# Performance work log

Measured on AMD Instinct MI355X. Metric: run time of the kernel, lower is better.

## Reference

```python
import jax, jax.numpy as jnp
import numpy as np

N_NODES = 10000
N_EDGES = 320000
HIDDEN = 64
IN_NODE = 4
IN_EDGE = 2
N_LAYERS = 4
COORDS_WEIGHT = 1.0
EPS = 1e-8


def _linear_params(key, fan_in, fan_out, scale=None, bias=True):
    k1, k2 = jax.random.split(key)
    s = scale if scale is not None else 1.0 / np.sqrt(fan_in)
    w = jax.random.uniform(k1, (fan_in, fan_out), jnp.float32, -s, s)
    b = jax.random.uniform(k2, (fan_out,), jnp.float32, -s, s) if bias else None
    return w, b


def setup_inputs() -> dict:
    key = jax.random.key(0)
    ks = jax.random.split(key, 16)
    his = jax.random.normal(ks[0], (N_NODES, IN_NODE), jnp.float32)
    loc = jax.random.normal(ks[1], (N_NODES, 3), jnp.float32)
    vel = jax.random.normal(ks[2], (N_NODES, 3), jnp.float32)
    edges = jax.random.randint(ks[3], (2, N_EDGES), 0, N_NODES, jnp.int64)
    edge_attr = jax.random.normal(ks[4], (N_EDGES, IN_EDGE), jnp.float32)
    emb_w, emb_b = _linear_params(ks[5], IN_NODE, HIDDEN)
    # edge MLP: cat(h_i, h_j, radial, edge_attr) -> hidden -> hidden
    edge_in = 2 * HIDDEN + 1 + IN_EDGE
    edge_w1, edge_b1 = _linear_params(ks[6], edge_in, HIDDEN)
    edge_w2, edge_b2 = _linear_params(ks[7], HIDDEN, HIDDEN)
    # node MLP: cat(h, agg) -> hidden -> hidden
    node_w1, node_b1 = _linear_params(ks[8], 2 * HIDDEN, HIDDEN)
    node_w2, node_b2 = _linear_params(ks[9], HIDDEN, HIDDEN)
    # coord MLP: hidden -> hidden -> 1 (last layer xavier-small, no bias, as in EGNN)
    coord_w1, coord_b1 = _linear_params(ks[10], HIDDEN, HIDDEN)
    coord_w2 = jax.random.normal(ks[11], (HIDDEN, 1), jnp.float32) * 0.001
    # coord_mlp_vel: hidden -> hidden -> 1
    vel_w1, vel_b1 = _linear_params(ks[12], HIDDEN, HIDDEN)
    vel_w2, vel_b2 = _linear_params(ks[13], HIDDEN, 1)
    return dict(his=his, loc=loc, edges=edges, vel=vel, edge_attr=edge_attr,
                emb_w=emb_w, emb_b=emb_b,
                edge_w1=edge_w1, edge_b1=edge_b1, edge_w2=edge_w2, edge_b2=edge_b2,
                node_w1=node_w1, node_b1=node_b1, node_w2=node_w2, node_b2=node_b2,
                coord_w1=coord_w1, coord_b1=coord_b1, coord_w2=coord_w2,
                vel_w1=vel_w1, vel_b1=vel_b1, vel_w2=vel_w2, vel_b2=vel_b2)


def _segment_mean(data, seg, num_segments):
    s = jax.ops.segment_sum(data, seg, num_segments=num_segments)
    cnt = jax.ops.segment_sum(jnp.ones((data.shape[0], 1), data.dtype), seg, num_segments=num_segments)
    return s / jnp.clip(cnt, 1.0, None)


def _egcl_vel(h, row, col, coord, vel, init_vel, edge_attr, p):
    """One E_GCL_ERGN_vel call: equivariant message passing + 2nd-order update."""
    n = h.shape[0]
    coord_diff = coord[row] - coord[col]                       # [E,3]
    radial = jnp.sum(coord_diff * coord_diff, axis=-1, keepdims=True)  # [E,1]
    # edge model
    e_in = jnp.concatenate([h[row], h[col], radial, edge_attr], axis=-1)
    ef = jax.nn.silu(e_in @ p['edge_w1'] + p['edge_b1'])
    ef = jax.nn.silu(ef @ p['edge_w2'] + p['edge_b2'])         # [E,H]
    # coord (acceleration) model
    gate = jax.nn.silu(ef @ p['coord_w1'] + p['coord_b1']) @ p['coord_w2']  # [E,1]
    acc = _segment_mean(coord_diff * gate, row, n) * COORDS_WEIGHT          # [N,3]
    # velocity model (norm_vel=True: normalize initial velocity direction)
    iv = init_vel / (jnp.linalg.norm(init_vel, axis=-1, keepdims=True) + EPS)
    phi = jax.nn.silu(h @ p['vel_w1'] + p['vel_b1']) @ p['vel_w2'] + p['vel_b2']  # [N,1]
    vel_new = vel + acc + phi * iv
    coord_new = coord + vel_new
    # node model
    agg = jax.ops.segment_sum(ef, row, num_segments=n)         # [N,H]
    hn = jax.nn.silu(jnp.concatenate([h, agg], axis=-1) @ p['node_w1'] + p['node_b1'])
    hn = hn @ p['node_w2'] + p['node_b2']                      # recurrent=False
    return hn, coord_new, vel_new


def reference(his, loc, edges, vel, edge_attr,
              emb_w, emb_b,
              edge_w1, edge_b1, edge_w2, edge_b2,
              node_w1, node_b1, node_w2, node_b2,
              coord_w1, coord_b1, coord_w2,
              vel_w1, vel_b1, vel_w2, vel_b2):
    p = dict(edge_w1=edge_w1, edge_b1=edge_b1, edge_w2=edge_w2, edge_b2=edge_b2,
             node_w1=node_w1, node_b1=node_b1, node_w2=node_w2, node_b2=node_b2,
             coord_w1=coord_w1, coord_b1=coord_b1, coord_w2=coord_w2,
             vel_w1=vel_w1, vel_b1=vel_b1, vel_w2=vel_w2, vel_b2=vel_b2)
    row, col = edges[0], edges[1]
    his_e = his @ emb_w + emb_b                                # embedding
    hi, x, v = _egcl_vel(his_e, row, col, loc, vel, vel, edge_attr, p)
    h = his_e + hi                                             # residual accumulation
    for _ in range(1, N_LAYERS):                               # shared layer, n_layers iters
        hi, x, v = _egcl_vel(h, row, col, x, v, vel, edge_attr, p)
        h = h + hi
    return x, h, v


if __name__ == '__main__':
    out = reference(**setup_inputs())
    print([o.shape for o in out])
```

## Files before the change

kernel.cpp:

```cpp
#include <hip/hip_runtime.h>
#include <hip/hip_bf16.h>
#include <math.h>

#define N_NODES 10000
#define N_EDGES 320000
#define HID 64
#define N_LAYERS 4
#define EDGE_BLOCKS 1250
#define EDGE_TILES_PER_WAVE 4
#define N_TILES_NODE 625
#define ALD 72

typedef unsigned short ushort_t;
typedef unsigned int uint_t;
typedef __attribute__((ext_vector_type(8))) short short8;
typedef __attribute__((ext_vector_type(4))) float floatx4;

__device__ __forceinline__ float silu_f(float x) {
    return x * (1.0f / (1.0f + __expf(-x)));
}
__device__ __forceinline__ ushort_t f2bf(float f) {
    uint_t u = __float_as_uint(f);
    uint_t r = u + 0x7FFFu + ((u >> 16) & 1u);
    return (ushort_t)(r >> 16);
}
__device__ __forceinline__ float bf2f(ushort_t u) {
    return __uint_as_float(((uint_t)u) << 16);
}
__device__ __forceinline__ uint_t pk2bf(float a, float b) {
    __hip_bfloat162 t = __float22bfloat162_rn(float2{a, b});
    union { __hip_bfloat162 h; uint_t u; } cv; cv.h = t; return cv.u;
}

__global__ void init_kernel(const float* __restrict__ loc, const float* __restrict__ vel,
                            float* __restrict__ x, float* __restrict__ v, float* __restrict__ iv) {
    int i = blockIdx.x * blockDim.x + threadIdx.x;
    if (i >= N_NODES) return;
    float v0 = vel[3*i], v1 = vel[3*i+1], v2 = vel[3*i+2];
    float nrm = sqrtf(v0*v0 + v1*v1 + v2*v2) + 1e-8f;
    x[3*i] = loc[3*i]; x[3*i+1] = loc[3*i+1]; x[3*i+2] = loc[3*i+2];
    v[3*i] = v0; v[3*i+1] = v1; v[3*i+2] = v2;
    iv[3*i] = v0/nrm; iv[3*i+1] = v1/nrm; iv[3*i+2] = v2/nrm;
}

__global__ __launch_bounds__(64) void embed_kernel(const float* __restrict__ his,
                                                   const float* __restrict__ w,
                                                   const float* __restrict__ b,
                                                   float* __restrict__ h0,
                                                   ushort_t* __restrict__ hbf) {
    int i = blockIdx.x, l = threadIdx.x;
    float acc = b[l];
    #pragma unroll
    for (int k = 0; k < 4; ++k) acc += his[i*4+k] * w[k*HID+l];
    h0[i*HID+l] = acc;
    hbf[i*HID+l] = f2bf(acc);
}

__global__ void count_kernel(const int* __restrict__ erow, int* __restrict__ counts) {
    int e = blockIdx.x * blockDim.x + threadIdx.x;
    if (e < N_EDGES) atomicAdd(&counts[erow[e]], 1);
}

__global__ __launch_bounds__(256) void scan_kernel(const int* __restrict__ counts,
                                                   int* __restrict__ offs) {
    __shared__ int part[256];
    const int t = threadIdx.x;
    const int base = t * 40;
    int s0 = 0;
    for (int k = 0; k < 40; ++k) {
        int i = base + k;
        if (i < N_NODES) s0 += counts[i];
    }
    part[t] = s0;
    __syncthreads();
    for (int d = 1; d < 256; d <<= 1) {
        int vv = (t >= d) ? part[t-d] : 0;
        __syncthreads();
        part[t] += vv;
        __syncthreads();
    }
    int run = part[t] - s0;
    for (int k = 0; k < 40; ++k) {
        int i = base + k;
        if (i < N_NODES) { run += counts[i]; offs[i+1] = run; }
    }
    if (t == 0) offs[0] = 0;
}

__global__ void scatter_kernel(const int* __restrict__ erow, const int* __restrict__ ecol,
                               const float* __restrict__ eattr,
                               const int* __restrict__ offs,
                               int* __restrict__ cursor,
                               int* __restrict__ srow, int* __restrict__ scol,
                               float* __restrict__ seattr) {
    int e = blockIdx.x * blockDim.x + threadIdx.x;
    if (e < N_EDGES) {
        int r = erow[e];
        int p = atomicAdd(&cursor[r], 1);
        int pos = offs[r] + p;
        srow[pos] = r;
        scol[pos] = ecol[e];
        seattr[2*pos]   = eattr[2*e];
        seattr[2*pos+1] = eattr[2*e+1];
    }
}

__device__ __forceinline__ void pack_one(const float* __restrict__ src, ushort_t* __restrict__ dst,
                                         int u) {
    int kt = u >> 8, nt = (u >> 6) & 3, lane = u & 63;
    int quad = lane >> 4, lo = lane & 15;
    #pragma unroll
    for (int j = 0; j < 8; ++j) {
        int k = 32*kt + quad*8 + j, n = 16*nt + lo;
        dst[(size_t)u*8 + j] = f2bf(src[k*HID + n]);
    }
}
__global__ void pack_weights(const float* __restrict__ ew1, const float* __restrict__ ew2,
                             const float* __restrict__ cw1, const float* __restrict__ nw1,
                             const float* __restrict__ nw2, const float* __restrict__ vw1,
                             ushort_t* __restrict__ pw1, ushort_t* __restrict__ pw2,
                             ushort_t* __restrict__ pc1, ushort_t* __restrict__ pn1,
                             ushort_t* __restrict__ pn2, ushort_t* __restrict__ pv1) {
    int t = blockIdx.x * blockDim.x + threadIdx.x;
    if      (t < 1024) pack_one(ew1, pw1, t);
    else if (t < 1536) pack_one(ew2, pw2, t - 1024);
    else if (t < 2048) pack_one(cw1, pc1, t - 1536);
    else if (t < 3072) pack_one(nw1, pn1, t - 2048);
    else if (t < 3584) pack_one(nw2, pn2, t - 3072);
    else               pack_one(vw1, pv1, t - 3584);
}

__global__ __launch_bounds__(256, 4) void edge_kernel(
    const ushort_t* __restrict__ hbf, const float* __restrict__ x,
    const int* __restrict__ srow, const int* __restrict__ scol,
    const float* __restrict__ seattr,
    const float* __restrict__ ew1,
    const float* __restrict__ eb1, const float* __restrict__ eb2,
    const float* __restrict__ cb1, const float* __restrict__ cw2,
    const ushort_t* __restrict__ pw1, const ushort_t* __restrict__ pw2,
    const ushort_t* __restrict__ pc1,
    float* __restrict__ aggf, float* __restrict__ accf)
{
    __shared__ ushort_t sW1[4*4*64*8];
    __shared__ ushort_t sW2[2*4*64*8];
    __shared__ float sRW[3][HID];
    __shared__ float sB1[HID], sB2[HID], sCB1[HID], sCW2[HID];
    __shared__ ushort_t sAct[4][16*ALD];
    __shared__ float sEdge[4][16][8];

    const int wave = threadIdx.x >> 6, lane = threadIdx.x & 63;
    const int quad = lane >> 4, lo = lane & 15;

    short8 c1f[8];
    #pragma unroll
    for (int u = 0; u < 8; ++u)
        c1f[u] = *(const short8*)(pc1 + ((size_t)u*64 + lane)*8);

    for (int i = threadIdx.x; i < 4*4*64*8; i += 256) sW1[i] = pw1[i];
    for (int i = threadIdx.x; i < 2*4*64*8; i += 256) sW2[i] = pw2[i];
    for (int i = threadIdx.x; i < 3*HID; i += 256) sRW[i/HID][i%HID] = ew1[(128 + i/HID)*HID + (i%HID)];
    if (threadIdx.x < HID) {
        sB1[threadIdx.x]  = eb1[threadIdx.x];
        sB2[threadIdx.x]  = eb2[threadIdx.x];
        sCB1[threadIdx.x] = cb1[threadIdx.x];
        sCW2[threadIdx.x] = cw2[threadIdx.x];
    }
    __syncthreads();

    ushort_t* act = sAct[wave];
    float (*sed)[8] = sEdge[wave];

    int tile = blockIdx.x * 4 + wave;
    for (int it = 0; it < EDGE_TILES_PER_WAVE; ++it, tile += EDGE_BLOCKS*4) {
        const int p0 = tile * 16;
        const int rme = srow[p0 + lo], cme = scol[p0 + lo];
        if (lane < 16) {
            float d0 = x[3*rme]   - x[3*cme];
            float d1 = x[3*rme+1] - x[3*cme+1];
            float d2 = x[3*rme+2] - x[3*cme+2];
            const float2 ea = ((const float2*)seattr)[p0 + lane];
            sed[lane][0] = d0; sed[lane][1] = d1; sed[lane][2] = d2;
            sed[lane][3] = d0*d0 + d1*d1 + d2*d2;
            sed[lane][4] = ea.x; sed[lane][5] = ea.y;
        }
        const int nxt = __shfl(rme, (lane + 1) & 63, 64);
        unsigned long long bm = __ballot((lane < 16) && ((lane == 15) || (rme != nxt)));
        const uint_t bnd = (uint_t)(bm & 0xFFFFu);

        const ushort_t* hr = hbf + (size_t)rme * HID;
        const ushort_t* hc = hbf + (size_t)cme * HID;
        short8 af0 = *(const short8*)(hr + quad*8);
        short8 af1 = *(const short8*)(hr + 32 + quad*8);
        short8 af2 = *(const short8*)(hc + quad*8);
        short8 af3 = *(const short8*)(hc + 32 + quad*8);

        floatx4 acc[4];
        #pragma unroll
        for (int nt = 0; nt < 4; ++nt) {
            floatx4 a = {0.f, 0.f, 0.f, 0.f};
            a = __builtin_amdgcn_mfma_f32_16x16x32_bf16(af0, *(const short8*)(sW1 + ((0*4+nt)*64+lane)*8), a, 0, 0, 0);
            a = __builtin_amdgcn_mfma_f32_16x16x32_bf16(af1, *(const short8*)(sW1 + ((1*4+nt)*64+lane)*8), a, 0, 0, 0);
            a = __builtin_amdgcn_mfma_f32_16x16x32_bf16(af2, *(const short8*)(sW1 + ((2*4+nt)*64+lane)*8), a, 0, 0, 0);
            a = __builtin_amdgcn_mfma_f32_16x16x32_bf16(af3, *(const short8*)(sW1 + ((3*4+nt)*64+lane)*8), a, 0, 0, 0);
            acc[nt] = a;
        }
        float rad[4], ea0[4], ea1[4];
        #pragma unroll
        for (int r = 0; r < 4; ++r) {
            const int m = 4*quad + r;
            rad[r] = sed[m][3]; ea0[r] = sed[m][4]; ea1[r] = sed[m][5];
        }
        #pragma unroll
        for (int nt = 0; nt < 4; ++nt) {
            const int n = 16*nt + lo;
            const float w128 = sRW[0][n], w129 = sRW[1][n], w130 = sRW[2][n], b1 = sB1[n];
            float vv[4];
            #pragma unroll
            for (int r = 0; r < 4; ++r)
                vv[r] = silu_f(acc[nt][r] + rad[r]*w128 + ea0[r]*w129 + ea1[r]*w130 + b1);
            const uint_t p01 = pk2bf(vv[0], vv[1]);
            const uint_t p23 = pk2bf(vv[2], vv[3]);
            act[(4*quad + 0)*ALD + n] = (ushort_t)(p01 & 0xFFFFu);
            act[(4*quad + 1)*ALD + n] = (ushort_t)(p01 >> 16);
            act[(4*quad + 2)*ALD + n] = (ushort_t)(p23 & 0xFFFFu);
            act[(4*quad + 3)*ALD + n] = (ushort_t)(p23 >> 16);
        }

        short8 g0 = *(const short8*)(act + lo*ALD + quad*8);
        short8 g1 = *(const short8*)(act + lo*ALD + 32 + quad*8);
        floatx4 acc2[4];
        #pragma unroll
        for (int nt = 0; nt < 4; ++nt) {
            floatx4 a = {0.f, 0.f, 0.f, 0.f};
            a = __builtin_amdgcn_mfma_f32_16x16x32_bf16(g0, *(const short8*)(sW2 + ((0*4+nt)*64+lane)*8), a, 0, 0, 0);
            a = __builtin_amdgcn_mfma_f32_16x16x32_bf16(g1, *(const short8*)(sW2 + ((1*4+nt)*64+lane)*8), a, 0, 0, 0);
            acc2[nt] = a;
        }
        #pragma unroll
        for (int nt = 0; nt < 4; ++nt) {
            const int n = 16*nt + lo;
            const float b2 = sB2[n];
            float vv[4];
            #pragma unroll
            for (int r = 0; r < 4; ++r) vv[r] = silu_f(acc2[nt][r] + b2);
            const uint_t p01 = pk2bf(vv[0], vv[1]);
            const uint_t p23 = pk2bf(vv[2], vv[3]);
            act[(4*quad + 0)*ALD + n] = (ushort_t)(p01 & 0xFFFFu);
            act[(4*quad + 1)*ALD + n] = (ushort_t)(p01 >> 16);
            act[(4*quad + 2)*ALD + n] = (ushort_t)(p23 & 0xFFFFu);
            act[(4*quad + 3)*ALD + n] = (ushort_t)(p23 >> 16);
        }

        {
            float s = 0.f;
            #pragma unroll
            for (int m = 0; m < 16; ++m) {
                s += bf2f(act[m*ALD + lane]);
                if ((bnd >> m) & 1u) {
                    const int row = __shfl(rme, m, 64);
                    atomicAdd(&aggf[(size_t)row*HID + lane], s);
                    s = 0.f;
                }
            }
        }

        short8 q0 = *(const short8*)(act + lo*ALD + quad*8);
        short8 q1 = *(const short8*)(act + lo*ALD + 32 + quad*8);
        float gs[4] = {0.f, 0.f, 0.f, 0.f};
        #pragma unroll
        for (int nt = 0; nt < 4; ++nt) {
            floatx4 a = {0.f, 0.f, 0.f, 0.f};
            a = __builtin_amdgcn_mfma_f32_16x16x32_bf16(q0, c1f[0*4+nt], a, 0, 0, 0);
            a = __builtin_amdgcn_mfma_f32_16x16x32_bf16(q1, c1f[1*4+nt], a, 0, 0, 0);
            const int n = 16*nt + lo;
            const float cb = sCB1[n], cw = sCW2[n];
            #pragma unroll
            for (int r = 0; r < 4; ++r) gs[r] += silu_f(a[r] + cb) * cw;
        }
        #pragma unroll
        for (int off = 1; off < 16; off <<= 1) {
            #pragma unroll
            for (int r = 0; r < 4; ++r) gs[r] += __shfl_xor(gs[r], off, 64);
        }
        int rr[4];
        #pragma unroll
        for (int r = 0; r < 4; ++r) rr[r] = __shfl(rme, 4*quad + r, 64);
        if (lo < 3) {
            #pragma unroll
            for (int r = 0; r < 4; ++r) {
                const int m = 4*quad + r;
                atomicAdd(&accf[(size_t)rr[r]*3 + lo], sed[m][lo] * gs[r]);
            }
        }
        __syncthreads();
    }
}

__global__ __launch_bounds__(64) void node_kernel(
    const float* __restrict__ h_in, float* __restrict__ h_out, ushort_t* __restrict__ hbf,
    float* __restrict__ x, float* __restrict__ v, const float* __restrict__ iv,
    float* __restrict__ aggf, float* __restrict__ accf,
    const int* __restrict__ offs,
    const ushort_t* __restrict__ pn1, const ushort_t* __restrict__ pn2,
    const ushort_t* __restrict__ pv1,
    const float* __restrict__ nb1, const float* __restrict__ nb2,
    const float* __restrict__ vb1, const float* __restrict__ vb2,
    const float* __restrict__ vw2)
{
    __shared__ ushort_t t1[16*ALD];
    __shared__ float sPhi[16];

    const int lane = threadIdx.x;
    const int tile = blockIdx.x;
    const int quad = lane >> 4, lo = lane & 15;
    const int i0 = tile * 16;

    int ov = 0;
    if (lane < 17) ov = offs[i0 + lane];

    const ushort_t* hrow = hbf + (size_t)(i0 + lo) * HID;
    short8 af0 = *(const short8*)(hrow + quad*8);
    short8 af1 = *(const short8*)(hrow + 32 + quad*8);
    float* ag = aggf + (size_t)(i0 + lo) * HID + quad*8;
    short8 af2, af3;
    #pragma unroll
    for (int j = 0; j < 4; ++j) {
        const uint_t u2 = pk2bf(ag[2*j], ag[2*j+1]);
        const uint_t u3 = pk2bf(ag[32 + 2*j], ag[32 + 2*j+1]);
        af2[2*j] = (short)(u2 & 0xFFFFu); af2[2*j+1] = (short)(u2 >> 16);
        af3[2*j] = (short)(u3 & 0xFFFFu); af3[2*j+1] = (short)(u3 >> 16);
    }
    floatx4 z = {0.f, 0.f, 0.f, 0.f};
    *(floatx4*)(ag)        = z;
    *(floatx4*)(ag + 4)    = z;
    *(floatx4*)(ag + 32)   = z;
    *(floatx4*)(ag + 36)   = z;

    #pragma unroll
    for (int nt = 0; nt < 4; ++nt) {
        floatx4 a = {0.f, 0.f, 0.f, 0.f};
        a = __builtin_amdgcn_mfma_f32_16x16x32_bf16(af0, *(const short8*)(pn1 + ((size_t)(0*4+nt)*64+lane)*8), a, 0, 0, 0);
        a = __builtin_amdgcn_mfma_f32_16x16x32_bf16(af1, *(const short8*)(pn1 + ((size_t)(1*4+nt)*64+lane)*8), a, 0, 0, 0);
        a = __builtin_amdgcn_mfma_f32_16x16x32_bf16(af2, *(const short8*)(pn1 + ((size_t)(2*4+nt)*64+lane)*8), a, 0, 0, 0);
        a = __builtin_amdgcn_mfma_f32_16x16x32_bf16(af3, *(const short8*)(pn1 + ((size_t)(3*4+nt)*64+lane)*8), a, 0, 0, 0);
        const int n = 16*nt + lo;
        const float b1 = nb1[n];
        float vv[4];
        #pragma unroll
        for (int r = 0; r < 4; ++r) vv[r] = silu_f(a[r] + b1);
        const uint_t p01 = pk2bf(vv[0], vv[1]);
        const uint_t p23 = pk2bf(vv[2], vv[3]);
        t1[(4*quad + 0)*ALD + n] = (ushort_t)(p01 & 0xFFFFu);
        t1[(4*quad + 1)*ALD + n] = (ushort_t)(p01 >> 16);
        t1[(4*quad + 2)*ALD + n] = (ushort_t)(p23 & 0xFFFFu);
        t1[(4*quad + 3)*ALD + n] = (ushort_t)(p23 >> 16);
    }

    short8 g0 = *(const short8*)(t1 + lo*ALD + quad*8);
    short8 g1 = *(const short8*)(t1 + lo*ALD + 32 + quad*8);
    #pragma unroll
    for (int nt = 0; nt < 4; ++nt) {
        floatx4 a = {0.f, 0.f, 0.f, 0.f};
        a = __builtin_amdgcn_mfma_f32_16x16x32_bf16(g0, *(const short8*)(pn2 + ((size_t)(0*4+nt)*64+lane)*8), a, 0, 0, 0);
        a = __builtin_amdgcn_mfma_f32_16x16x32_bf16(g1, *(const short8*)(pn2 + ((size_t)(1*4+nt)*64+lane)*8), a, 0, 0, 0);
        const int n = 16*nt + lo;
        const float b2 = nb2[n];
        #pragma unroll
        for (int r = 0; r < 4; ++r) {
            const int i = i0 + 4*quad + r;
            const float hnew = h_in[(size_t)i*HID + n] + a[r] + b2;
            h_out[(size_t)i*HID + n] = hnew;
            hbf[(size_t)i*HID + n] = f2bf(hnew);
        }
    }

    float gs[4] = {0.f, 0.f, 0.f, 0.f};
    #pragma unroll
    for (int nt = 0; nt < 4; ++nt) {
        floatx4 a = {0.f, 0.f, 0.f, 0.f};
        a = __builtin_amdgcn_mfma_f32_16x16x32_bf16(af0, *(const short8*)(pv1 + ((size_t)(0*4+nt)*64+lane)*8), a, 0, 0, 0);
        a = __builtin_amdgcn_mfma_f32_16x16x32_bf16(af1, *(const short8*)(pv1 + ((size_t)(1*4+nt)*64+lane)*8), a, 0, 0, 0);
        const int n = 16*nt + lo;
        const float b1 = vb1[n], w2 = vw2[n];
        #pragma unroll
        for (int r = 0; r < 4; ++r) gs[r] += silu_f(a[r] + b1) * w2;
    }
    #pragma unroll
    for (int off = 1; off < 16; off <<= 1) {
        #pragma unroll
        for (int r = 0; r < 4; ++r) gs[r] += __shfl_xor(gs[r], off, 64);
    }
    const float vb2s = vb2[0];
    if (lo == 0) {
        #pragma unroll
        for (int r = 0; r < 4; ++r) sPhi[4*quad + r] = gs[r] + vb2s;
    }

    if (lane < 48) {
        const int m = lane / 3, d = lane - m*3;
        const int s = __shfl(ov, m, 64), t = __shfl(ov, m + 1, 64);
        const int cnt = t - s;
        const int i = i0 + m;
        const float accm = accf[(size_t)i*3 + d] / (float)(cnt > 0 ? cnt : 1);
        accf[(size_t)i*3 + d] = 0.f;
        const float phi = sPhi[m];
        const float vn = v[3*i + d] + accm + phi * iv[3*i + d];
        v[3*i + d] = vn;
        x[3*i + d] += vn;
    }
}

__global__ void out_kernel(const float* __restrict__ x, const float* __restrict__ h,
                           const float* __restrict__ v, float* __restrict__ out) {
    int j = blockIdx.x * blockDim.x + threadIdx.x;
    const int nx = 3*N_NODES, nh = HID*N_NODES;
    if (j >= nx + nh + nx) return;
    if (j < nx) out[j] = x[j];
    else if (j < nx + nh) out[j] = h[j - nx];
    else out[j] = v[j - nx - nh];
}

extern "C" void kernel_launch(void* const* d_in, const int* in_sizes, int n_in,
                              void* d_out, int out_size, void* d_ws, size_t ws_size,
                              hipStream_t stream) {
    const float* his   = (const float*)d_in[0];
    const float* loc   = (const float*)d_in[1];
    const int*   edges = (const int*)  d_in[2];
    const float* vel   = (const float*)d_in[3];
    const float* eattr = (const float*)d_in[4];
    const float* emb_w = (const float*)d_in[5];
    const float* emb_b = (const float*)d_in[6];
    const float* ew1 = (const float*)d_in[7];
    const float* eb1 = (const float*)d_in[8];
    const float* ew2 = (const float*)d_in[9];
    const float* eb2 = (const float*)d_in[10];
    const float* nw1 = (const float*)d_in[11];
    const float* nb1 = (const float*)d_in[12];
    const float* nw2 = (const float*)d_in[13];
    const float* nb2 = (const float*)d_in[14];
    const float* cw1 = (const float*)d_in[15];
    const float* cb1 = (const float*)d_in[16];
    const float* cw2 = (const float*)d_in[17];
    const float* vw1 = (const float*)d_in[18];
    const float* vb1 = (const float*)d_in[19];
    const float* vw2 = (const float*)d_in[20];
    const float* vb2 = (const float*)d_in[21];

    const int* erow = edges;
    const int* ecol = edges + N_EDGES;

    char* ws = (char*)d_ws;
    size_t off = 0;
    auto walloc = [&](size_t bytes) -> void* {
        void* p = ws + off; off += (bytes + 255) & ~(size_t)255; return p;
    };
    float* h_a      = (float*)walloc((size_t)N_NODES*HID*4);
    float* h_b      = (float*)walloc((size_t)N_NODES*HID*4);
    ushort_t* hbf   = (ushort_t*)walloc((size_t)N_NODES*HID*2);
    float* xb       = (float*)walloc((size_t)N_NODES*3*4);
    float* vb       = (float*)walloc((size_t)N_NODES*3*4);
    float* ivb      = (float*)walloc((size_t)N_NODES*3*4);
    float* aggf     = (float*)walloc((size_t)N_NODES*HID*4);
    float* accf     = (float*)walloc((size_t)N_NODES*3*4);
    int* counts     = (int*)walloc((size_t)N_NODES*4);
    int* cursor     = (int*)walloc((size_t)N_NODES*4);
    int* offs       = (int*)walloc((size_t)(N_NODES+1)*4);
    int* srow       = (int*)walloc((size_t)N_EDGES*4);
    int* scol       = (int*)walloc((size_t)N_EDGES*4);
    float* seattr   = (float*)walloc((size_t)N_EDGES*2*4);
    ushort_t* pw1   = (ushort_t*)walloc((size_t)4*4*64*8*2);
    ushort_t* pw2   = (ushort_t*)walloc((size_t)2*4*64*8*2);
    ushort_t* pc1   = (ushort_t*)walloc((size_t)2*4*64*8*2);
    ushort_t* pn1   = (ushort_t*)walloc((size_t)4*4*64*8*2);
    ushort_t* pn2   = (ushort_t*)walloc((size_t)2*4*64*8*2);
    ushort_t* pv1   = (ushort_t*)walloc((size_t)2*4*64*8*2);

    (void)hipMemsetAsync(counts, 0, (size_t)N_NODES*4, stream);
    (void)hipMemsetAsync(cursor, 0, (size_t)N_NODES*4, stream);
    (void)hipMemsetAsync(aggf, 0, (size_t)N_NODES*HID*4, stream);
    (void)hipMemsetAsync(accf, 0, (size_t)N_NODES*3*4, stream);

    init_kernel<<<(N_NODES+255)/256, 256, 0, stream>>>(loc, vel, xb, vb, ivb);
    embed_kernel<<<N_NODES, 64, 0, stream>>>(his, emb_w, emb_b, h_a, hbf);
    count_kernel<<<(N_EDGES+255)/256, 256, 0, stream>>>(erow, counts);
    scan_kernel<<<1, 256, 0, stream>>>(counts, offs);
    scatter_kernel<<<(N_EDGES+255)/256, 256, 0, stream>>>(erow, ecol, eattr, offs, cursor,
                                                          srow, scol, seattr);
    pack_weights<<<16, 256, 0, stream>>>(ew1, ew2, cw1, nw1, nw2, vw1,
                                         pw1, pw2, pc1, pn1, pn2, pv1);

    float* h_cur = h_a;
    float* h_nxt = h_b;
    for (int layer = 0; layer < N_LAYERS; ++layer) {
        edge_kernel<<<EDGE_BLOCKS, 256, 0, stream>>>(hbf, xb, srow, scol, seattr,
                                                     ew1, eb1, eb2, cb1, cw2,
                                                     pw1, pw2, pc1, aggf, accf);
        node_kernel<<<N_TILES_NODE, 64, 0, stream>>>(h_cur, h_nxt, hbf, xb, vb, ivb,
                                                     aggf, accf, offs,
                                                     pn1, pn2, pv1,
                                                     nb1, nb2, vb1, vb2, vw2);
        float* tmp = h_cur; h_cur = h_nxt; h_nxt = tmp;
    }
    const int total = 3*N_NODES + HID*N_NODES + 3*N_NODES;
    out_kernel<<<(total+255)/256, 256, 0, stream>>>(xb, h_cur, vb, (float*)d_out);
}
```

Baseline: 499.1 us.

## Keep W2 in registers, raise edge occupancy, fuse init and output kernels

The edge kernel now holds the second-layer weights in per-lane registers instead of LDS, which shrinks shared memory. It raises the launch-bounds occupancy hint to 5 and pads the grid to 1280 blocks, adding a bounds guard per tile. Separately, the init kernel is merged into the embedding kernel, and the final node kernel writes x, h and v straight into the output buffer, so the out_kernel copy is gone. The cost is higher register pressure in the edge kernel, and some waves do no work because of the padded grid.

Result: slower. 542.3 us (+8.6%).

```diff
diff --git a/kernel.cpp b/kernel.cpp
--- a/kernel.cpp
+++ b/kernel.cpp
@@ -6,8 +6,9 @@
 #define N_EDGES 320000
 #define HID 64
 #define N_LAYERS 4
-#define EDGE_BLOCKS 1250
+#define EDGE_BLOCKS 1280
 #define EDGE_TILES_PER_WAVE 4
+#define N_TILES_EDGE 20000
 #define N_TILES_NODE 625
 #define ALD 72
 
@@ -32,28 +33,28 @@
     union { __hip_bfloat162 h; uint_t u; } cv; cv.h = t; return cv.u;
 }
 
-__global__ void init_kernel(const float* __restrict__ loc, const float* __restrict__ vel,
-                            float* __restrict__ x, float* __restrict__ v, float* __restrict__ iv) {
-    int i = blockIdx.x * blockDim.x + threadIdx.x;
-    if (i >= N_NODES) return;
-    float v0 = vel[3*i], v1 = vel[3*i+1], v2 = vel[3*i+2];
-    float nrm = sqrtf(v0*v0 + v1*v1 + v2*v2) + 1e-8f;
-    x[3*i] = loc[3*i]; x[3*i+1] = loc[3*i+1]; x[3*i+2] = loc[3*i+2];
-    v[3*i] = v0; v[3*i+1] = v1; v[3*i+2] = v2;
-    iv[3*i] = v0/nrm; iv[3*i+1] = v1/nrm; iv[3*i+2] = v2/nrm;
-}
-
 __global__ __launch_bounds__(64) void embed_kernel(const float* __restrict__ his,
+                                                   const float* __restrict__ loc,
+                                                   const float* __restrict__ vel,
                                                    const float* __restrict__ w,
                                                    const float* __restrict__ b,
                                                    float* __restrict__ h0,
-                                                   ushort_t* __restrict__ hbf) {
+                                                   ushort_t* __restrict__ hbf,
+                                                   float* __restrict__ x, float* __restrict__ v,
+                                                   float* __restrict__ iv) {
     int i = blockIdx.x, l = threadIdx.x;
     float acc = b[l];
     #pragma unroll
     for (int k = 0; k < 4; ++k) acc += his[i*4+k] * w[k*HID+l];
     h0[i*HID+l] = acc;
     hbf[i*HID+l] = f2bf(acc);
+    if (l == 0) {
+        float v0 = vel[3*i], v1 = vel[3*i+1], v2 = vel[3*i+2];
+        float nrm = sqrtf(v0*v0 + v1*v1 + v2*v2) + 1e-8f;
+        x[3*i] = loc[3*i]; x[3*i+1] = loc[3*i+1]; x[3*i+2] = loc[3*i+2];
+        v[3*i] = v0; v[3*i+1] = v1; v[3*i+2] = v2;
+        iv[3*i] = v0/nrm; iv[3*i+1] = v1/nrm; iv[3*i+2] = v2/nrm;
+    }
 }
 
 __global__ void count_kernel(const int* __restrict__ erow, int* __restrict__ counts) {
@@ -130,7 +131,7 @@
     else               pack_one(vw1, pv1, t - 3584);
 }
 
-__global__ __launch_bounds__(256, 4) void edge_kernel(
+__global__ __launch_bounds__(256, 5) void edge_kernel(
     const ushort_t* __restrict__ hbf, const float* __restrict__ x,
     const int* __restrict__ srow, const int* __restrict__ scol,
     const float* __restrict__ seattr,
@@ -142,7 +143,6 @@
     float* __restrict__ aggf, float* __restrict__ accf)
 {
     __shared__ ushort_t sW1[4*4*64*8];
-    __shared__ ushort_t sW2[2*4*64*8];
     __shared__ float sRW[3][HID];
     __shared__ float sB1[HID], sB2[HID], sCB1[HID], sCW2[HID];
     __shared__ ushort_t sAct[4][16*ALD];
@@ -151,13 +151,14 @@
     const int wave = threadIdx.x >> 6, lane = threadIdx.x & 63;
     const int quad = lane >> 4, lo = lane & 15;
 
-    short8 c1f[8];
-    #pragma unroll
-    for (int u = 0; u < 8; ++u)
+    short8 w2f[8], c1f[8];
+    #pragma unroll
+    for (int u = 0; u < 8; ++u) {
+        w2f[u] = *(const short8*)(pw2 + ((size_t)u*64 + lane)*8);
         c1f[u] = *(const short8*)(pc1 + ((size_t)u*64 + lane)*8);
+    }
 
     for (int i = threadIdx.x; i < 4*4*64*8; i += 256) sW1[i] = pw1[i];
-    for (int i = threadIdx.x; i < 2*4*64*8; i += 256) sW2[i] = pw2[i];
     for (int i = threadIdx.x; i < 3*HID; i += 256) sRW[i/HID][i%HID] = ew1[(128 + i/HID)*HID + (i%HID)];
     if (threadIdx.x < HID) {
         sB1[threadIdx.x]  = eb1[threadIdx.x];
@@ -172,124 +173,126 @@
 
     int tile = blockIdx.x * 4 + wave;
     for (int it = 0; it < EDGE_TILES_PER_WAVE; ++it, tile += EDGE_BLOCKS*4) {
-        const int p0 = tile * 16;
-        const int rme = srow[p0 + lo], cme = scol[p0 + lo];
-        if (lane < 16) {
-            float d0 = x[3*rme]   - x[3*cme];
-            float d1 = x[3*rme+1] - x[3*cme+1];
-            float d2 = x[3*rme+2] - x[3*cme+2];
-            const float2 ea = ((const float2*)seattr)[p0 + lane];
-            sed[lane][0] = d0; sed[lane][1] = d1; sed[lane][2] = d2;
-            sed[lane][3] = d0*d0 + d1*d1 + d2*d2;
-            sed[lane][4] = ea.x; sed[lane][5] = ea.y;
-        }
-        const int nxt = __shfl(rme, (lane + 1) & 63, 64);
-        unsigned long long bm = __ballot((lane < 16) && ((lane == 15) || (rme != nxt)));
-        const uint_t bnd = (uint_t)(bm & 0xFFFFu);
-
-        const ushort_t* hr = hbf + (size_t)rme * HID;
-        const ushort_t* hc = hbf + (size_t)cme * HID;
-        short8 af0 = *(const short8*)(hr + quad*8);
-        short8 af1 = *(const short8*)(hr + 32 + quad*8);
-        short8 af2 = *(const short8*)(hc + quad*8);
-        short8 af3 = *(const short8*)(hc + 32 + quad*8);
-
-        floatx4 acc[4];
-        #pragma unroll
-        for (int nt = 0; nt < 4; ++nt) {
-            floatx4 a = {0.f, 0.f, 0.f, 0.f};
-            a = __builtin_amdgcn_mfma_f32_16x16x32_bf16(af0, *(const short8*)(sW1 + ((0*4+nt)*64+lane)*8), a, 0, 0, 0);
-            a = __builtin_amdgcn_mfma_f32_16x16x32_bf16(af1, *(const short8*)(sW1 + ((1*4+nt)*64+lane)*8), a, 0, 0, 0);
-            a = __builtin_amdgcn_mfma_f32_16x16x32_bf16(af2, *(const short8*)(sW1 + ((2*4+nt)*64+lane)*8), a, 0, 0, 0);
-            a = __builtin_amdgcn_mfma_f32_16x16x32_bf16(af3, *(const short8*)(sW1 + ((3*4+nt)*64+lane)*8), a, 0, 0, 0);
-            acc[nt] = a;
-        }
-        float rad[4], ea0[4], ea1[4];
-        #pragma unroll
-        for (int r = 0; r < 4; ++r) {
-            const int m = 4*quad + r;
-            rad[r] = sed[m][3]; ea0[r] = sed[m][4]; ea1[r] = sed[m][5];
-        }
-        #pragma unroll
-        for (int nt = 0; nt < 4; ++nt) {
-            const int n = 16*nt + lo;
-            const float w128 = sRW[0][n], w129 = sRW[1][n], w130 = sRW[2][n], b1 = sB1[n];
-            float vv[4];
-            #pragma unroll
-            for (int r = 0; r < 4; ++r)
-                vv[r] = silu_f(acc[nt][r] + rad[r]*w128 + ea0[r]*w129 + ea1[r]*w130 + b1);
-            const uint_t p01 = pk2bf(vv[0], vv[1]);
-            const uint_t p23 = pk2bf(vv[2], vv[3]);
-            act[(4*quad + 0)*ALD + n] = (ushort_t)(p01 & 0xFFFFu);
-            act[(4*quad + 1)*ALD + n] = (ushort_t)(p01 >> 16);
-            act[(4*quad + 2)*ALD + n] = (ushort_t)(p23 & 0xFFFFu);
-            act[(4*quad + 3)*ALD + n] = (ushort_t)(p23 >> 16);
-        }
-
-        short8 g0 = *(const short8*)(act + lo*ALD + quad*8);
-        short8 g1 = *(const short8*)(act + lo*ALD + 32 + quad*8);
-        floatx4 acc2[4];
-        #pragma unroll
-        for (int nt = 0; nt < 4; ++nt) {
-            floatx4 a = {0.f, 0.f, 0.f, 0.f};
-            a = __builtin_amdgcn_mfma_f32_16x16x32_bf16(g0, *(const short8*)(sW2 + ((0*4+nt)*64+lane)*8), a, 0, 0, 0);
-            a = __builtin_amdgcn_mfma_f32_16x16x32_bf16(g1, *(const short8*)(sW2 + ((1*4+nt)*64+lane)*8), a, 0, 0, 0);
-            acc2[nt] = a;
-        }
-        #pragma unroll
-        for (int nt = 0; nt < 4; ++nt) {
-            const int n = 16*nt + lo;
-            const float b2 = sB2[n];
-            float vv[4];
-            #pragma unroll
-            for (int r = 0; r < 4; ++r) vv[r] = silu_f(acc2[nt][r] + b2);
-            const uint_t p01 = pk2bf(vv[0], vv[1]);
-            const uint_t p23 = pk2bf(vv[2], vv[3]);
-            act[(4*quad + 0)*ALD + n] = (ushort_t)(p01 & 0xFFFFu);
-            act[(4*quad + 1)*ALD + n] = (ushort_t)(p01 >> 16);
-            act[(4*quad + 2)*ALD + n] = (ushort_t)(p23 & 0xFFFFu);
-            act[(4*quad + 3)*ALD + n] = (ushort_t)(p23 >> 16);
-        }
-
-        {
-            float s = 0.f;
-            #pragma unroll
-            for (int m = 0; m < 16; ++m) {
-                s += bf2f(act[m*ALD + lane]);
-                if ((bnd >> m) & 1u) {
-                    const int row = __shfl(rme, m, 64);
-                    atomicAdd(&aggf[(size_t)row*HID + lane], s);
-                    s = 0.f;
-                }
-            }
-        }
-
-        short8 q0 = *(const short8*)(act + lo*ALD + quad*8);
-        short8 q1 = *(const short8*)(act + lo*ALD + 32 + quad*8);
-        float gs[4] = {0.f, 0.f, 0.f, 0.f};
-        #pragma unroll
-        for (int nt = 0; nt < 4; ++nt) {
-            floatx4 a = {0.f, 0.f, 0.f, 0.f};
-            a = __builtin_amdgcn_mfma_f32_16x16x32_bf16(q0, c1f[0*4+nt], a, 0, 0, 0);
-            a = __builtin_amdgcn_mfma_f32_16x16x32_bf16(q1, c1f[1*4+nt], a, 0, 0, 0);
-            const int n = 16*nt + lo;
-            const float cb = sCB1[n], cw = sCW2[n];
-            #pragma unroll
-            for (int r = 0; r < 4; ++r) gs[r] += silu_f(a[r] + cb) * cw;
-        }
-        #pragma unroll
-        for (int off = 1; off < 16; off <<= 1) {
-            #pragma unroll
-            for (int r = 0; r < 4; ++r) gs[r] += __shfl_xor(gs[r], off, 64);
-        }
-        int rr[4];
-        #pragma unroll
-        for (int r = 0; r < 4; ++r) rr[r] = __shfl(rme, 4*quad + r, 64);
-        if (lo < 3) {
+        if (tile < N_TILES_EDGE) {
+            const int p0 = tile * 16;
+            const int rme = srow[p0 + lo], cme = scol[p0 + lo];
+            if (lane < 16) {
+                float d0 = x[3*rme]   - x[3*cme];
+                float d1 = x[3*rme+1] - x[3*cme+1];
+                float d2 = x[3*rme+2] - x[3*cme+2];
+                const float2 ea = ((const float2*)seattr)[p0 + lane];
+                sed[lane][0] = d0; sed[lane][1] = d1; sed[lane][2] = d2;
+                sed[lane][3] = d0*d0 + d1*d1 + d2*d2;
+                sed[lane][4] = ea.x; sed[lane][5] = ea.y;
+            }
+            const int nxt = __shfl(rme, (lane + 1) & 63, 64);
+            unsigned long long bm = __ballot((lane < 16) && ((lane == 15) || (rme != nxt)));
+            const uint_t bnd = (uint_t)(bm & 0xFFFFu);
+
+            const ushort_t* hr = hbf + (size_t)rme * HID;
+            const ushort_t* hc = hbf + (size_t)cme * HID;
+            short8 af0 = *(const short8*)(hr + quad*8);
+            short8 af1 = *(const short8*)(hr + 32 + quad*8);
+            short8 af2 = *(const short8*)(hc + quad*8);
+            short8 af3 = *(const short8*)(hc + 32 + quad*8);
+
+            floatx4 acc[4];
+            #pragma unroll
+            for (int nt = 0; nt < 4; ++nt) {
+                floatx4 a = {0.f, 0.f, 0.f, 0.f};
+                a = __builtin_amdgcn_mfma_f32_16x16x32_bf16(af0, *(const short8*)(sW1 + ((0*4+nt)*64+lane)*8), a, 0, 0, 0);
+                a = __builtin_amdgcn_mfma_f32_16x16x32_bf16(af1, *(const short8*)(sW1 + ((1*4+nt)*64+lane)*8), a, 0, 0, 0);
+                a = __builtin_amdgcn_mfma_f32_16x16x32_bf16(af2, *(const short8*)(sW1 + ((2*4+nt)*64+lane)*8), a, 0, 0, 0);
+                a = __builtin_amdgcn_mfma_f32_16x16x32_bf16(af3, *(const short8*)(sW1 + ((3*4+nt)*64+lane)*8), a, 0, 0, 0);
+                acc[nt] = a;
+            }
+            float rad[4], ea0[4], ea1[4];
             #pragma unroll
             for (int r = 0; r < 4; ++r) {
                 const int m = 4*quad + r;
-                atomicAdd(&accf[(size_t)rr[r]*3 + lo], sed[m][lo] * gs[r]);
+                rad[r] = sed[m][3]; ea0[r] = sed[m][4]; ea1[r] = sed[m][5];
+            }
+            #pragma unroll
+            for (int nt = 0; nt < 4; ++nt) {
+                const int n = 16*nt + lo;
+                const float w128 = sRW[0][n], w129 = sRW[1][n], w130 = sRW[2][n], b1 = sB1[n];
+                float vv[4];
+                #pragma unroll
+                for (int r = 0; r < 4; ++r)
+                    vv[r] = silu_f(acc[nt][r] + rad[r]*w128 + ea0[r]*w129 + ea1[r]*w130 + b1);
+                const uint_t p01 = pk2bf(vv[0], vv[1]);
+                const uint_t p23 = pk2bf(vv[2], vv[3]);
+                act[(4*quad + 0)*ALD + n] = (ushort_t)(p01 & 0xFFFFu);
+                act[(4*quad + 1)*ALD + n] = (ushort_t)(p01 >> 16);
+                act[(4*quad + 2)*ALD + n] = (ushort_t)(p23 & 0xFFFFu);
+                act[(4*quad + 3)*ALD + n] = (ushort_t)(p23 >> 16);
+            }
+
+            short8 g0 = *(const short8*)(act + lo*ALD + quad*8);
+            short8 g1 = *(const short8*)(act + lo*ALD + 32 + quad*8);
+            floatx4 acc2[4];
+            #pragma unroll
+            for (int nt = 0; nt < 4; ++nt) {
+                floatx4 a = {0.f, 0.f, 0.f, 0.f};
+                a = __builtin_amdgcn_mfma_f32_16x16x32_bf16(g0, w2f[0*4+nt], a, 0, 0, 0);
+                a = __builtin_amdgcn_mfma_f32_16x16x32_bf16(g1, w2f[1*4+nt], a, 0, 0, 0);
+                acc2[nt] = a;
+            }
+            #pragma unroll
+            for (int nt = 0; nt < 4; ++nt) {
+                const int n = 16*nt + lo;
+                const float b2 = sB2[n];
+                float vv[4];
+                #pragma unroll
+                for (int r = 0; r < 4; ++r) vv[r] = silu_f(acc2[nt][r] + b2);
+                const uint_t p01 = pk2bf(vv[0], vv[1]);
+                const uint_t p23 = pk2bf(vv[2], vv[3]);
+                act[(4*quad + 0)*ALD + n] = (ushort_t)(p01 & 0xFFFFu);
+                act[(4*quad + 1)*ALD + n] = (ushort_t)(p01 >> 16);
+                act[(4*quad + 2)*ALD + n] = (ushort_t)(p23 & 0xFFFFu);
+                act[(4*quad + 3)*ALD + n] = (ushort_t)(p23 >> 16);
+            }
+
+            {
+                float s = 0.f;
+                #pragma unroll
+                for (int m = 0; m < 16; ++m) {
+                    s += bf2f(act[m*ALD + lane]);
+                    if ((bnd >> m) & 1u) {
+                        const int row = __shfl(rme, m, 64);
+                        atomicAdd(&aggf[(size_t)row*HID + lane], s);
+                        s = 0.f;
+                    }
+                }
+            }
+
+            short8 q0 = *(const short8*)(act + lo*ALD + quad*8);
+            short8 q1 = *(const short8*)(act + lo*ALD + 32 + quad*8);
+            float gs[4] = {0.f, 0.f, 0.f, 0.f};
+            #pragma unroll
+            for (int nt = 0; nt < 4; ++nt) {
+                floatx4 a = {0.f, 0.f, 0.f, 0.f};
+                a = __builtin_amdgcn_mfma_f32_16x16x32_bf16(q0, c1f[0*4+nt], a, 0, 0, 0);
+                a = __builtin_amdgcn_mfma_f32_16x16x32_bf16(q1, c1f[1*4+nt], a, 0, 0, 0);
+                const int n = 16*nt + lo;
+                const float cb = sCB1[n], cw = sCW2[n];
+                #pragma unroll
+                for (int r = 0; r < 4; ++r) gs[r] += silu_f(a[r] + cb) * cw;
+            }
+            #pragma unroll
+            for (int off = 1; off < 16; off <<= 1) {
+                #pragma unroll
+                for (int r = 0; r < 4; ++r) gs[r] += __shfl_xor(gs[r], off, 64);
+            }
+            int rr[4];
+            #pragma unroll
+            for (int r = 0; r < 4; ++r) rr[r] = __shfl(rme, 4*quad + r, 64);
+            if (lo < 3) {
+                #pragma unroll
+                for (int r = 0; r < 4; ++r) {
+                    const int m = 4*quad + r;
+                    atomicAdd(&accf[(size_t)rr[r]*3 + lo], sed[m][lo] * gs[r]);
+                }
             }
         }
         __syncthreads();
@@ -305,7 +308,8 @@
     const ushort_t* __restrict__ pv1,
     const float* __restrict__ nb1, const float* __restrict__ nb2,
     const float* __restrict__ vb1, const float* __restrict__ vb2,
-    const float* __restrict__ vw2)
+    const float* __restrict__ vw2,
+    float* __restrict__ outx, float* __restrict__ outv)
 {
     __shared__ ushort_t t1[16*ALD];
     __shared__ float sPhi[16];
@@ -331,10 +335,10 @@
         af3[2*j] = (short)(u3 & 0xFFFFu); af3[2*j+1] = (short)(u3 >> 16);
     }
     floatx4 z = {0.f, 0.f, 0.f, 0.f};
-    *(floatx4*)(ag)        = z;
-    *(floatx4*)(ag + 4)    = z;
-    *(floatx4*)(ag + 32)   = z;
-    *(floatx4*)(ag + 36)   = z;
+    *(floatx4*)(ag)      = z;
+    *(floatx4*)(ag + 4)  = z;
+    *(floatx4*)(ag + 32) = z;
+    *(floatx4*)(ag + 36) = z;
 
     #pragma unroll
     for (int nt = 0; nt < 4; ++nt) {
@@ -405,19 +409,14 @@
         accf[(size_t)i*3 + d] = 0.f;
         const float phi = sPhi[m];
         const float vn = v[3*i + d] + accm + phi * iv[3*i + d];
+        const float xn = x[3*i + d] + vn;
         v[3*i + d] = vn;
-        x[3*i + d] += vn;
-    }
-}
-
-__global__ void out_kernel(const float* __restrict__ x, const float* __restrict__ h,
-                           const float* __restrict__ v, float* __restrict__ out) {
-    int j = blockIdx.x * blockDim.x + threadIdx.x;
-    const int nx = 3*N_NODES, nh = HID*N_NODES;
-    if (j >= nx + nh + nx) return;
-    if (j < nx) out[j] = x[j];
-    else if (j < nx + nh) out[j] = h[j - nx];
-    else out[j] = v[j - nx - nh];
+        x[3*i + d] = xn;
+        if (outx) {
+            outx[3*i + d] = xn;
+            outv[3*i + d] = vn;
+        }
+    }
 }
 
 extern "C" void kernel_launch(void* const* d_in, const int* in_sizes, int n_in,
@@ -475,13 +474,16 @@
     ushort_t* pn2   = (ushort_t*)walloc((size_t)2*4*64*8*2);
     ushort_t* pv1   = (ushort_t*)walloc((size_t)2*4*64*8*2);
 
+    float* out = (float*)d_out;
+    const int nx = 3*N_NODES, nh = HID*N_NODES;
+
     (void)hipMemsetAsync(counts, 0, (size_t)N_NODES*4, stream);
     (void)hipMemsetAsync(cursor, 0, (size_t)N_NODES*4, stream);
     (void)hipMemsetAsync(aggf, 0, (size_t)N_NODES*HID*4, stream);
     (void)hipMemsetAsync(accf, 0, (size_t)N_NODES*3*4, stream);
 
-    init_kernel<<<(N_NODES+255)/256, 256, 0, stream>>>(loc, vel, xb, vb, ivb);
-    embed_kernel<<<N_NODES, 64, 0, stream>>>(his, emb_w, emb_b, h_a, hbf);
+    embed_kernel<<<N_NODES, 64, 0, stream>>>(his, loc, vel, emb_w, emb_b, h_a, hbf,
+                                             xb, vb, ivb);
     count_kernel<<<(N_EDGES+255)/256, 256, 0, stream>>>(erow, counts);
     scan_kernel<<<1, 256, 0, stream>>>(counts, offs);
     scatter_kernel<<<(N_EDGES+255)/256, 256, 0, stream>>>(erow, ecol, eattr, offs, cursor,
@@ -492,15 +494,18 @@
     float* h_cur = h_a;
     float* h_nxt = h_b;
     for (int layer = 0; layer < N_LAYERS; ++layer) {
+        const bool last = (layer == N_LAYERS - 1);
         edge_kernel<<<EDGE_BLOCKS, 256, 0, stream>>>(hbf, xb, srow, scol, seattr,
                                                      ew1, eb1, eb2, cb1, cw2,
                                                      pw1, pw2, pc1, aggf, accf);
-        node_kernel<<<N_TILES_NODE, 64, 0, stream>>>(h_cur, h_nxt, hbf, xb, vb, ivb,
+        node_kernel<<<N_TILES_NODE, 64, 0, stream>>>(h_cur,
+                                                     last ? (out + nx) : h_nxt,
+                                                     hbf, xb, vb, ivb,
                                                      aggf, accf, offs,
                                                      pn1, pn2, pv1,
-                                                     nb1, nb2, vb1, vb2, vw2);
+                                                     nb1, nb2, vb1, vb2, vw2,
+                                                     last ? out : nullptr,
+                                                     last ? (out + nx + nh) : nullptr);
         float* tmp = h_cur; h_cur = h_nxt; h_nxt = tmp;
     }
-    const int total = 3*N_NODES + HID*N_NODES + 3*N_NODES;
-    out_kernel<<<(total+255)/256, 256, 0, stream>>>(xb, h_cur, vb, (float*)d_out);
-}
+}
```
